# Kernel optimization log

Hardware: AMD Instinct MI355X
Metric: run time of the kernel (lower is better)

The kernel has to match this reference:

```python
import jax, jax.numpy as jnp
import numpy as np

D_MODEL = 256
GAMMA = 0.9          # ret_D is built in the torch forward but never applied to the output; kept for fidelity notes
SCALE_BASE = 512     # XPOS default
TEMP = 10000.0
TWO_PI = 2.0 * np.pi


def sine_pos_embed(x):
    """DETR-style 1D sine position embedding with an all-ones mask (as in forward).
    x: [B,T,C] -> pos: [1,T,C] (mask is [1,T] ones, so batch dim broadcasts)."""
    T, C = x.shape[1], x.shape[2]
    x_embed = jnp.arange(1, T + 1, dtype=jnp.float32)          # cumsum of ones
    x_embed = x_embed / (x_embed[-1] + 1e-6) * TWO_PI          # normalize=True
    dim_t = TEMP ** (2.0 * (jnp.arange(C) // 2).astype(jnp.float32) / C)
    pos = x_embed[:, None] / dim_t                             # [T,C]
    pos = jnp.stack([jnp.sin(pos[:, 0::2]), jnp.cos(pos[:, 1::2])], axis=2).reshape(T, C)
    return pos[None].astype(x.dtype)


def _dup_interleave(m):
    # [L, d/2] -> [L, d], columns repeated pairwise: [a,b] -> [a,a,b,b]
    return jnp.repeat(m, 2, axis=-1)


def _rotate_every_two(x):
    x1, x2 = x[..., 0::2], x[..., 1::2]
    return jnp.stack([-x2, x1], axis=-1).reshape(x.shape)


def xpos_apply(x, downscale=False):
    """RetNet XPOS rotary embedding. x: [B,L,d]."""
    L, d = x.shape[1], x.shape[2]
    half = d // 2
    scale_vec = (jnp.arange(0, d, 2, dtype=jnp.float32) + 0.4 * d) / (1.4 * d)   # [d/2]
    power = jnp.arange(L, dtype=jnp.float32) / SCALE_BASE
    scale = scale_vec[None, :] ** power[:, None]                                  # [L, d/2]
    inv_freq = 1.0 / (TEMP ** (jnp.arange(half, dtype=jnp.float32) / half))
    sinusoid = jnp.arange(L, dtype=jnp.float32)[:, None] * inv_freq[None, :]      # [L, d/2]
    sin, cos = jnp.sin(sinusoid), jnp.cos(sinusoid)
    if downscale:
        scale = 1.0 / scale
    sin_s = _dup_interleave(sin * scale)[None].astype(x.dtype)   # [1,L,d]
    cos_s = _dup_interleave(cos * scale)[None].astype(x.dtype)
    return x * cos_s + _rotate_every_two(x) * sin_s


def setup_inputs() -> dict:
    key = jax.random.key(0)
    ks = jax.random.split(key, 8)
    B, TXT, VID, D = 16, 32, 2048, D_MODEL
    S = TXT + VID
    inp = {
        "src": jax.random.normal(ks[0], (B, S, D), dtype=jnp.float32),
        "learn_vid_ret": jax.random.normal(ks[1], (VID * VID, 1), dtype=jnp.float32),
        "W_txt_Q": jax.random.normal(ks[2], (D, D), dtype=jnp.float32) / D,
        "W_txt_K": jax.random.normal(ks[3], (D, D), dtype=jnp.float32) / D,
        "W_txt_V": jax.random.normal(ks[4], (D, D), dtype=jnp.float32) / D,
        "W_vid_Q": jax.random.normal(ks[5], (D, D), dtype=jnp.float32) / D,
        "W_vid_K": jax.random.normal(ks[6], (D, D), dtype=jnp.float32) / D,
        "W_vid_V": jax.random.normal(ks[7], (D, D), dtype=jnp.float32) / D,
        "txt_length": TXT,
    }
    return inp


def reference(src, learn_vid_ret, W_txt_Q, W_txt_K, W_txt_V, W_vid_Q, W_vid_K, W_vid_V, txt_length):
    S = src.shape[1]
    vid_length = S - txt_length

    # learned retention mask over the video block
    learn_ret = jax.nn.sigmoid(learn_vid_ret.reshape(vid_length, vid_length))
    diag = jnp.eye(vid_length, dtype=src.dtype)
    video_ret = (1.0 - diag) * learn_ret
    loss_sparsity = jnp.mean(jnp.abs(video_ret))

    # full [S,S] mask: ones everywhere, sigmoid(learned) on the vid-vid block
    ret_mask = jnp.ones((S, S), dtype=src.dtype).at[txt_length:, txt_length:].set(learn_ret)

    txt_mem = src[:, :txt_length]   # [B,TXT,D]
    vid_mem = src[:, txt_length:]   # [B,VID,D]

    pos = sine_pos_embed(txt_mem)   # [1,TXT,D]
    txt_Q = (pos + txt_mem) @ W_txt_Q
    txt_K = (pos + txt_mem) @ W_txt_K
    vid_Q = xpos_apply(vid_mem @ W_vid_Q)
    vid_K = xpos_apply(vid_mem @ W_vid_K, downscale=True)

    Q = jnp.concatenate([txt_Q, vid_Q], axis=1)                  # [B,S,D]
    K = jnp.concatenate([txt_K, vid_K], axis=1)                  # [B,S,D]
    V = jnp.concatenate([txt_mem @ W_txt_V, vid_mem @ W_vid_V], axis=1)

    # retention: QK^T elementwise-masked (no softmax), then weighted V sum
    scores = jnp.einsum('bsd,btd->bst', Q, K) * ret_mask[None]   # [B,S,S]
    out = scores @ V                                             # [B,S,D]
    return out, loss_sparsity
```

## Files before the change

### kernel.cpp

```cpp
#include <hip/hip_runtime.h>

#define B_   16
#define TXT  32
#define VID  2048
#define D_   256
#define S_   2080
#define SP   2176
#define NKT  34
#define GTOT 17424

typedef unsigned short ushort_t;
typedef __attribute__((ext_vector_type(8))) short short8;
typedef __attribute__((ext_vector_type(4))) short short4v;
typedef __attribute__((ext_vector_type(4))) float f32x4;
typedef __attribute__((ext_vector_type(16))) float f32x16;

__device__ __forceinline__ ushort_t f2bf(float f) {
  unsigned u = __builtin_bit_cast(unsigned, f);
  unsigned r = (u + 0x7FFFu + ((u >> 16) & 1u)) >> 16;
  return (ushort_t)r;
}
__device__ __forceinline__ float bf2f(ushort_t h) {
  unsigned u = ((unsigned)h) << 16;
  return __builtin_bit_cast(float, u);
}

__device__ __forceinline__ void g2l16(void* lds, const void* g) {
  __builtin_amdgcn_global_load_lds(
      (const __attribute__((address_space(1))) char*)g,
      (__attribute__((address_space(3))) char*)lds, 16, 0, 0);
}

__device__ __forceinline__ f32x4 mfma16(short8 a, short8 b, f32x4 c) {
  return __builtin_amdgcn_mfma_f32_16x16x32_bf16(a, b, c, 0, 0, 0);
}
__device__ __forceinline__ f32x16 mfma32(short8 a, short8 b, f32x16 c) {
  return __builtin_amdgcn_mfma_f32_32x32x16_bf16(a, b, c, 0, 0, 0);
}


__global__ void tbl_kernel(float* __restrict__ tbl) {
  int idx = blockIdx.x * 256 + threadIdx.x;
  int n = idx >> 7, i = idx & 127;
  float invf = powf(10000.0f, -(float)i / 128.0f);
  float ang = (float)n * invf;
  float s, co;
  sincosf(ang, &s, &co);
  float sv = ((float)(2 * i) + 102.4f) / 358.4f;
  float sc = powf(sv, (float)n / 512.0f);
  float4 r;
  r.x = co * sc; r.y = s * sc; r.z = co / sc; r.w = s / sc;
  *(float4*)(tbl + (size_t)idx * 4) = r;
}

__global__ void sig_loss_kernel(const float* __restrict__ learn, ushort_t* __restrict__ sigp,
                                float* __restrict__ loss) {
  const int tid = threadIdx.x;
  const int base = (blockIdx.x * 256 + tid) * 8;
  float4 v0 = *(const float4*)(learn + base);
  float4 v1 = *(const float4*)(learn + base + 4);
  float vals[8] = {v0.x, v0.y, v0.z, v0.w, v1.x, v1.y, v1.z, v1.w};
  float acc = 0.f;
  short8 sh;
  #pragma unroll
  for (int j = 0; j < 8; ++j) {
    int idx = base + j;
    float s = 1.0f / (1.0f + expf(-vals[j]));
    sh[j] = (short)f2bf(s);
    int rr = idx >> 11, cc = idx & 2047;
    if (rr != cc) acc += s;
  }
  *(short8*)(sigp + base) = sh;
  __shared__ float red[256];
  red[tid] = acc;
  __syncthreads();
  #pragma unroll
  for (int st = 128; st > 0; st >>= 1) {
    if (tid < st) red[tid] += red[tid + st];
    __syncthreads();
  }
  if (tid == 0) atomicAdd(loss, red[0] * (1.0f / 4194304.0f));
}

__global__ void cvt_kernel(const float* __restrict__ src, ushort_t* __restrict__ srcb) {
  int i = blockIdx.x * 256 + threadIdx.x;
  int b = i >> 16;
  int rem = i & 65535;
  int row = rem >> 5, c8 = (rem & 31) * 8;
  const float* p = src + ((size_t)b * S_ + TXT + row) * D_ + c8;
  float4 v0 = *(const float4*)p;
  float4 v1 = *(const float4*)(p + 4);
  short8 h;
  h[0] = (short)f2bf(v0.x); h[1] = (short)f2bf(v0.y); h[2] = (short)f2bf(v0.z); h[3] = (short)f2bf(v0.w);
  h[4] = (short)f2bf(v1.x); h[5] = (short)f2bf(v1.y); h[6] = (short)f2bf(v1.z); h[7] = (short)f2bf(v1.w);
  *(short8*)(srcb + ((size_t)b * VID + row) * D_ + c8) = h;
}

__global__ void pad0_kernel(ushort_t* __restrict__ Qs, ushort_t* __restrict__ Ks,
                            ushort_t* __restrict__ VTs) {
  int i = blockIdx.x * 256 + threadIdx.x;
  short8 z = {0, 0, 0, 0, 0, 0, 0, 0};
  int sec = i >> 14;
  int j = i & 16383;
  int bb = j >> 10;
  int rem = j & 1023;
  size_t base = ((size_t)(bb * NKT + 32)) << 14;
  if (sec == 0) {
    int kstep = rem >> 6, ch = rem & 63;
    *(short8*)(Qs + base + kstep * 1024 + 512 + ch * 8) = z;
  } else if (sec == 1) {
    int kstep = rem >> 6, ch = rem & 63;
    *(short8*)(Ks + base + kstep * 1024 + 512 + ch * 8) = z;
  } else {
    *(short8*)(VTs + base + 8192 + rem * 8) = z;
  }
}

__global__ void wt_kernel(const float* __restrict__ Wq, const float* __restrict__ Wk,
                          const float* __restrict__ Wv, ushort_t* __restrict__ WT) {
  __shared__ float t[64][68];
  const int k0 = blockIdx.x * 64, n0 = blockIdx.y * 64, mt = blockIdx.z;
  const float* W = (mt == 0) ? Wq : (mt == 1) ? Wk : Wv;
  int tid = threadIdx.x;
  int r = tid >> 4, cq = (tid & 15) * 4;
  #pragma unroll
  for (int m = 0; m < 4; ++m) {
    int k = m * 16 + r;
    float4 v = *(const float4*)(W + (size_t)(k0 + k) * 256 + n0 + cq);
    t[k][cq] = v.x; t[k][cq + 1] = v.y; t[k][cq + 2] = v.z; t[k][cq + 3] = v.w;
  }
  __syncthreads();
  #pragma unroll
  for (int m = 0; m < 4; ++m) {
    int n = m * 16 + r;
    short4v h;
    h[0] = (short)f2bf(t[cq + 0][n]);
    h[1] = (short)f2bf(t[cq + 1][n]);
    h[2] = (short)f2bf(t[cq + 2][n]);
    h[3] = (short)f2bf(t[cq + 3][n]);
    *(short4v*)(WT + ((size_t)mt * D_ + n0 + n) * D_ + k0 + cq) = h;
  }
}

__global__ void txt_kernel(const float* __restrict__ src,
                           const float* __restrict__ Wq, const float* __restrict__ Wk,
                           const float* __restrict__ Wv,
                           ushort_t* __restrict__ Qs, ushort_t* __restrict__ Ks,
                           ushort_t* __restrict__ VTs) {
  __shared__ float a_s[8][256];
  __shared__ float x_s[8][256];
  const int tg = blockIdx.x;
  const int b  = blockIdx.y;
  const int c  = threadIdx.x;
  #pragma unroll
  for (int t = 0; t < 8; ++t) {
    int row = tg * 8 + t;
    float x = src[((size_t)b * S_ + row) * D_ + c];
    float xe = (float)(row + 1) * (6.283185307179586f / (32.0f + 1e-6f));
    int i = c >> 1;
    float dimt = powf(10000.0f, (2.0f * (float)i) / 256.0f);
    float ang = xe / dimt;
    float pv = (c & 1) ? cosf(ang) : sinf(ang);
    x_s[t][c] = x;
    a_s[t][c] = x + pv;
  }
  __syncthreads();
  float q[8] = {0,0,0,0,0,0,0,0}, k[8] = {0,0,0,0,0,0,0,0}, v[8] = {0,0,0,0,0,0,0,0};
  for (int kk = 0; kk < 256; ++kk) {
    float wq = Wq[(size_t)kk * 256 + c];
    float wk = Wk[(size_t)kk * 256 + c];
    float wv = Wv[(size_t)kk * 256 + c];
    #pragma unroll
    for (int t = 0; t < 8; ++t) {
      q[t] = fmaf(a_s[t][kk], wq, q[t]);
      k[t] = fmaf(a_s[t][kk], wk, k[t]);
      v[t] = fmaf(x_s[t][kk], wv, v[t]);
    }
  }
  #pragma unroll
  for (int t = 0; t < 8; ++t) {
    int row = tg * 8 + t;
    size_t base = ((size_t)(b * NKT)) << 14;
    size_t sub = (size_t)(c >> 4) * 1024 + row * 16 + (c & 15);
    Qs[base + sub] = f2bf(q[t]);
    Ks[base + sub] = f2bf(k[t]);
    VTs[base + (size_t)(row >> 4) * 4096 + c * 16 + (row & 15)] = f2bf(v[t]);
  }
}

template <int MODE>
__global__ __launch_bounds__(256, 2) void vid_gemm(
    const float* __restrict__ src, const ushort_t* __restrict__ srcb,
    const ushort_t* __restrict__ WT, const float* __restrict__ tbl,
    ushort_t* __restrict__ Qs, ushort_t* __restrict__ Ks, ushort_t* __restrict__ VTs) {
  __shared__ __align__(16) ushort_t ldsA[64 * 64];
  __shared__ __align__(16) ushort_t ldsB[64 * 64];

  const int rt = blockIdx.x;
  const int b  = blockIdx.y;
  const int ct = blockIdx.z;
  const int nt = ct >> 2;
  const int n0 = (ct & 3) * 64;
  const int tid = threadIdx.x;
  const int wv = tid >> 6, lane = tid & 63, l15 = lane & 15, l4 = lane >> 4;

  f32x4 acc[4];
  #pragma unroll
  for (int t2 = 0; t2 < 4; ++t2) { acc[t2][0] = 0.f; acc[t2][1] = 0.f; acc[t2][2] = 0.f; acc[t2][3] = 0.f; }

  for (int kk = 0; kk < 256; kk += 64) {
    if (MODE == 1) {
      #pragma unroll
      for (int m = 0; m < 2; ++m) {
        int p = (m * 256 + tid) * 16;
        int r = p >> 7;
        int cb = (p & 127) ^ ((r & 7) << 4);
        g2l16((char*)ldsA + p,
              (const char*)(srcb + ((size_t)b * VID + rt * 64 + r) * D_ + kk) + cb);
      }
    } else {
      #pragma unroll
      for (int m = 0; m < 4; ++m) {
        int q = m * 256 + tid;
        int r = q >> 4;
        int kc = (q & 15) * 4;
        const float4 v = *(const float4*)(src + ((size_t)b * S_ + TXT + rt * 64 + r) * D_ + kk + kc);
        short4v h;
        h[0] = (short)f2bf(v.x); h[1] = (short)f2bf(v.y);
        h[2] = (short)f2bf(v.z); h[3] = (short)f2bf(v.w);
        int off = ((r << 7) + (kc << 1)) ^ ((r & 7) << 4);
        *(short4v*)((char*)ldsA + off) = h;
      }
    }
    #pragma unroll
    for (int m = 0; m < 2; ++m) {
      int p = (m * 256 + tid) * 16;
      int nl = p >> 7;
      int c = (p & 127) ^ ((nl & 7) << 4);
      g2l16((char*)ldsB + p, (const char*)(WT + ((size_t)nt * D_ + n0 + nl) * D_ + kk) + c);
    }
    __syncthreads();
    #pragma unroll
    for (int ks = 0; ks < 2; ++ks) {
      int ar = wv * 16 + l15;
      int aoff = ((ar << 7) + ((ks * 32 + l4 * 8) << 1)) ^ ((ar & 7) << 4);
      short8 av = *(const short8*)((const char*)ldsA + aoff);
      #pragma unroll
      for (int t2 = 0; t2 < 4; ++t2) {
        int nl = t2 * 16 + l15;
        int boff = ((nl << 7) + ((ks * 32 + l4 * 8) << 1)) ^ ((nl & 7) << 4);
        short8 bv = *(const short8*)((const char*)ldsB + boff);
        acc[t2] = mfma16(av, bv, acc[t2]);
      }
    }
    __syncthreads();
  }

  const int rowl = wv * 16 + l4 * 4;
  if (nt < 2) {
    #pragma unroll
    for (int t2 = 0; t2 < 4; ++t2) {
      int c = n0 + t2 * 16 + l15;
      #pragma unroll
      for (int r = 0; r < 4; ++r) {
        int n = rt * 64 + rowl + r;
        float x = acc[t2][r];
        float xp = __shfl_xor(x, 1);
        const float4 tb = *(const float4*)(tbl + ((size_t)n * 128 + (c >> 1)) * 4);
        float cs = (nt == 0) ? tb.x : tb.z;
        float ss = (nt == 0) ? tb.y : tb.w;
        float val = (c & 1) ? fmaf(x, cs, xp * ss) : fmaf(x, cs, -xp * ss);
        int rowg = TXT + n;
        size_t idx = (((size_t)(b * NKT + (rowg >> 6))) << 14)
                   + (size_t)(c >> 4) * 1024 + (rowg & 63) * 16 + (c & 15);
        if (nt == 0) Qs[idx] = f2bf(val);
        else         Ks[idx] = f2bf(val);
      }
    }
  } else {
    #pragma unroll
    for (int t2 = 0; t2 < 4; ++t2)
      #pragma unroll
      for (int r = 0; r < 4; ++r) {
        int rr = rowl + r;
        int cc = t2 * 16 + l15;
        int off = ((rr << 7) + (cc << 1)) ^ ((rr & 7) << 4);
        *(ushort_t*)((char*)ldsA + off) = f2bf(acc[t2][r]);
      }
    __syncthreads();
    int n = tid >> 2;
    int rc = (tid & 3) * 16;
    short8 o0, o1;
    #pragma unroll
    for (int j = 0; j < 8; ++j) {
      int rr = rc + j;
      int off = ((rr << 7) + (n << 1)) ^ ((rr & 7) << 4);
      o0[j] = *(const short*)((const char*)ldsA + off);
    }
    #pragma unroll
    for (int j = 0; j < 8; ++j) {
      int rr = rc + 8 + j;
      int off = ((rr << 7) + (n << 1)) ^ ((rr & 7) << 4);
      o1[j] = *(const short*)((const char*)ldsA + off);
    }
    int d = n0 + n;
    int kvg0 = TXT + rt * 64 + rc;
    size_t base = (((size_t)(b * NKT + (kvg0 >> 6))) << 14) + ((kvg0 >> 4) & 3) * 4096 + d * 16;
    *(short8*)(VTs + base) = o0;
    *(short8*)(VTs + base + 8) = o1;
  }
}

__global__ __launch_bounds__(256) void attn_kernel(
    const ushort_t* __restrict__ Qs, const ushort_t* __restrict__ Ks,
    const ushort_t* __restrict__ VTs, const ushort_t* __restrict__ sigp,
    float* __restrict__ out) {
  __shared__ __align__(16) ushort_t Pb[4096];

  const int kblk = blockIdx.x;
  const int bs = (kblk & 7) * 128 + (kblk >> 3);
  int g = bs * 17 + (bs >> 6);
  const int gend = (bs + 1) * 17 + ((bs + 1) >> 6);

  const int tid = threadIdx.x;
  const int wid = tid >> 6, lane = tid & 63;
  const int l31 = lane & 31, l5 = lane >> 5;
  const int qh = wid >> 1, kh = wid & 1;
  const int d0 = wid * 64;
  const int qloc = qh * 32 + l31;
  const int pswz = (l31 & 7) << 4;

  int b = g / 1089, rem = g - b * 1089, qt = rem / 33, kvt = rem - qt * 33;

  f32x16 oacc[2][2];
  #pragma unroll
  for (int i2 = 0; i2 < 2; ++i2)
    #pragma unroll
    for (int j2 = 0; j2 < 2; ++j2)
      #pragma unroll
      for (int r = 0; r < 16; ++r) oacc[i2][j2][r] = 0.f;

  while (g < gend) {
    int4 mq[4];
    {
      int q = qt * 64 + qloc;
      int qc = q - TXT; qc = qc < 0 ? 0 : (qc > 2047 ? 2047 : qc);
      int kvp = kvt * 64 + kh * 32 - TXT;
      int kvc = (kvp >= 0 && kvp <= 2016) ? kvp : 0;
      const int4* mrow = (const int4*)(sigp + (size_t)qc * 2048 + kvc);
      mq[0] = mrow[0]; mq[1] = mrow[1]; mq[2] = mrow[2]; mq[3] = mrow[3];
    }

    const ushort_t* kb = Ks + (((size_t)(b * NKT + kvt)) << 14) + (kh * 32 + l31) * 16 + l5 * 8;
    const ushort_t* qb = Qs + (((size_t)(b * NKT + qt)) << 14) + qloc * 16 + l5 * 8;
    f32x16 s;
    #pragma unroll
    for (int r = 0; r < 16; ++r) s[r] = 0.f;
    __builtin_amdgcn_s_setprio(1);
    #pragma unroll
    for (int ks = 0; ks < 16; ++ks) {
      short8 kf = *(const short8*)(kb + ks * 1024);
      short8 qf = *(const short8*)(qb + ks * 1024);
      s = mfma32(kf, qf, s);
    }
    __builtin_amdgcn_s_setprio(0);

    {
      int q = qt * 64 + qloc;
      bool qv = (q >= TXT) && (q < S_);
      int kvp = kvt * 64 + kh * 32 - TXT;
      bool kvv = (kvp >= 0 && kvp <= 2016);
      bool ok = qv && kvv;
      const unsigned* mw = (const unsigned*)mq;
      #pragma unroll
      for (int t = 0; t < 4; ++t) {
        unsigned w0p, w1p;
        {
          unsigned wa = mw[4 * t + 0], wb = mw[4 * t + 2];
          unsigned w = l5 ? wb : wa;
          float m0 = ok ? bf2f((ushort_t)(w & 0xFFFFu)) : 1.0f;
          float m1 = ok ? bf2f((ushort_t)(w >> 16)) : 1.0f;
          int r = 4 * t;
          float p0 = s[r] * m0;
          float p1 = s[r + 1] * m1;
          asm("v_cvt_pk_bf16_f32 %0, %1, %2" : "=v"(w0p) : "v"(p0), "v"(p1));
        }
        {
          unsigned wa = mw[4 * t + 1], wb = mw[4 * t + 3];
          unsigned w = l5 ? wb : wa;
          float m0 = ok ? bf2f((ushort_t)(w & 0xFFFFu)) : 1.0f;
          float m1 = ok ? bf2f((ushort_t)(w >> 16)) : 1.0f;
          int r = 4 * t + 2;
          float p0 = s[r] * m0;
          float p1 = s[r + 1] * m1;
          asm("v_cvt_pk_bf16_f32 %0, %1, %2" : "=v"(w1p) : "v"(p0), "v"(p1));
        }
        int off = ((qloc << 7) + (kh << 6) + (t << 4) + (l5 << 3)) ^ pswz;
        *(uint2*)((char*)Pb + off) = make_uint2(w0p, w1p);
      }
    }

    asm volatile("s_waitcnt lgkmcnt(0)" ::: "memory");
    __builtin_amdgcn_sched_barrier(0);
    __builtin_amdgcn_s_barrier();
    __builtin_amdgcn_sched_barrier(0);

    const ushort_t* vb = VTs + (((size_t)(b * NKT + kvt)) << 14) + (size_t)d0 * 16 + l5 * 8;
    __builtin_amdgcn_s_setprio(1);
    #pragma unroll
    for (int ks = 0; ks < 4; ++ks) {
      short8 pf0 = *(const short8*)((const char*)Pb + ((l31 * 128 + ks * 32 + l5 * 16) ^ pswz));
      short8 pf1 = *(const short8*)((const char*)Pb + (((32 + l31) * 128 + ks * 32 + l5 * 16) ^ pswz));
      short8 vf0 = *(const short8*)(vb + ks * 4096 + l31 * 16);
      short8 vf1 = *(const short8*)(vb + ks * 4096 + (l31 + 32) * 16);
      oacc[0][0] = mfma32(pf0, vf0, oacc[0][0]);
      oacc[0][1] = mfma32(pf0, vf1, oacc[0][1]);
      oacc[1][0] = mfma32(pf1, vf0, oacc[1][0]);
      oacc[1][1] = mfma32(pf1, vf1, oacc[1][1]);
    }
    __builtin_amdgcn_s_setprio(0);
    asm volatile("s_waitcnt lgkmcnt(0)" ::: "memory");
    __builtin_amdgcn_sched_barrier(0);

    if (kvt == 32 || g + 1 == gend) {
      #pragma unroll
      for (int qg2 = 0; qg2 < 2; ++qg2)
        #pragma unroll
        for (int dg = 0; dg < 2; ++dg)
          #pragma unroll
          for (int r = 0; r < 16; ++r) {
            int qg = qt * 64 + qg2 * 32 + (r & 3) + 8 * (r >> 2) + 4 * l5;
            int dd = d0 + dg * 32 + l31;
            if (qg < S_)
              unsafeAtomicAdd(&out[((size_t)b * S_ + qg) * D_ + dd], oacc[qg2][dg][r]);
            oacc[qg2][dg][r] = 0.f;
          }
    }

    __builtin_amdgcn_s_barrier();
    __builtin_amdgcn_sched_barrier(0);

    ++g;
    ++kvt;
    if (kvt == 33) { kvt = 0; ++qt; if (qt == 33) { qt = 0; ++b; } }
  }
}

extern "C" void kernel_launch(void* const* d_in, const int* in_sizes, int n_in,
                              void* d_out, int out_size, void* d_ws, size_t ws_size,
                              hipStream_t stream) {
  (void)in_sizes; (void)n_in;
  const float* src   = (const float*)d_in[0];
  const float* learn = (const float*)d_in[1];
  const float* Wtq = (const float*)d_in[2];
  const float* Wtk = (const float*)d_in[3];
  const float* Wtv = (const float*)d_in[4];
  const float* Wvq = (const float*)d_in[5];
  const float* Wvk = (const float*)d_in[6];
  const float* Wvv = (const float*)d_in[7];
  float* out = (float*)d_out;

  char* ws = (char*)d_ws;
  const size_t QKV_ONE  = (size_t)B_ * SP * D_ * 2;
  const size_t QP_OFF   = 0;
  const size_t KS_OFF   = QP_OFF + QKV_ONE;
  const size_t VT_OFF   = KS_OFF + QKV_ONE;
  const size_t SIG_OFF  = VT_OFF + QKV_ONE;
  const size_t TBL_OFF  = SIG_OFF + (size_t)VID * VID * 2;
  const size_t WT_OFF   = TBL_OFF + (size_t)VID * 128 * 4 * sizeof(float);
  const size_t SRCB_OFF = WT_OFF + (size_t)3 * D_ * D_ * 2;
  const size_t NEED_SRCB = SRCB_OFF + (size_t)B_ * VID * D_ * 2;

  ushort_t* Qs   = (ushort_t*)(ws + QP_OFF);
  ushort_t* Ks   = (ushort_t*)(ws + KS_OFF);
  ushort_t* VTs  = (ushort_t*)(ws + VT_OFF);
  ushort_t* sigp = (ushort_t*)(ws + SIG_OFF);
  float*    tbl  = (float*)(ws + TBL_OFF);
  ushort_t* WT   = (ushort_t*)(ws + WT_OFF);
  ushort_t* srcb = (ushort_t*)(ws + SRCB_OFF);

  hipMemsetAsync(d_out, 0, (size_t)out_size * sizeof(float), stream);
  pad0_kernel<<<192, 256, 0, stream>>>(Qs, Ks, VTs);
  tbl_kernel<<<1024, 256, 0, stream>>>(tbl);
  sig_loss_kernel<<<2048, 256, 0, stream>>>(learn, sigp, out + (size_t)B_ * S_ * D_);
  wt_kernel<<<dim3(4, 4, 3), 256, 0, stream>>>(Wvq, Wvk, Wvv, WT);
  txt_kernel<<<dim3(4, B_), 256, 0, stream>>>(src, Wtq, Wtk, Wtv, Qs, Ks, VTs);
  if (ws_size >= NEED_SRCB) {
    cvt_kernel<<<4096, 256, 0, stream>>>(src, srcb);
    vid_gemm<1><<<dim3(32, B_, 12), 256, 0, stream>>>(src, srcb, WT, tbl, Qs, Ks, VTs);
  } else {
    vid_gemm<0><<<dim3(32, B_, 12), 256, 0, stream>>>(src, srcb, WT, tbl, Qs, Ks, VTs);
  }
  attn_kernel<<<dim3(1024), 256, 0, stream>>>(Qs, Ks, VTs, sigp, out);
}
```

Measured before the change: 356.8 us.

## Merge prep kernels, stage swizzled K tiles in LDS and prefetch next tile in attention

Five small preprocessing kernels (pad, table, sigmoid/loss, weight transpose, text projection) are folded into one launch to cut launch overhead. The K layout is XOR-swizzled on write. The attention kernel now stages each K tile into LDS with async global-to-LDS loads, keeps Q fragments in registers across kv tiles, and prefetches the next K tile, mask and Q while PV runs. The QK reduction is split into two independent accumulators, and the grid shrinks from 1024 to 768 blocks with more work each. This adds LDS use and register pressure, and relies on hand-counted vmcnt waits being correct.

```diff
diff --git a/kernel.cpp b/kernel.cpp
--- a/kernel.cpp
+++ b/kernel.cpp
@@ -39,47 +39,137 @@
 }
 
 
-__global__ void tbl_kernel(float* __restrict__ tbl) {
-  int idx = blockIdx.x * 256 + threadIdx.x;
-  int n = idx >> 7, i = idx & 127;
-  float invf = powf(10000.0f, -(float)i / 128.0f);
-  float ang = (float)n * invf;
-  float s, co;
-  sincosf(ang, &s, &co);
-  float sv = ((float)(2 * i) + 102.4f) / 358.4f;
-  float sc = powf(sv, (float)n / 512.0f);
-  float4 r;
-  r.x = co * sc; r.y = s * sc; r.z = co / sc; r.w = s / sc;
-  *(float4*)(tbl + (size_t)idx * 4) = r;
-}
-
-__global__ void sig_loss_kernel(const float* __restrict__ learn, ushort_t* __restrict__ sigp,
-                                float* __restrict__ loss) {
+__global__ void prep_kernel(const float* __restrict__ src, const float* __restrict__ learn,
+                            const float* __restrict__ Wtq, const float* __restrict__ Wtk,
+                            const float* __restrict__ Wtv,
+                            const float* __restrict__ Wvq, const float* __restrict__ Wvk,
+                            const float* __restrict__ Wvv,
+                            ushort_t* __restrict__ Qs, ushort_t* __restrict__ Ks,
+                            ushort_t* __restrict__ VTs, ushort_t* __restrict__ sigp,
+                            float* __restrict__ tbl, ushort_t* __restrict__ WT,
+                            float* __restrict__ loss) {
+  __shared__ float shf[64 * 68];
+  const int blk = blockIdx.x;
   const int tid = threadIdx.x;
-  const int base = (blockIdx.x * 256 + tid) * 8;
-  float4 v0 = *(const float4*)(learn + base);
-  float4 v1 = *(const float4*)(learn + base + 4);
-  float vals[8] = {v0.x, v0.y, v0.z, v0.w, v1.x, v1.y, v1.z, v1.w};
-  float acc = 0.f;
-  short8 sh;
-  #pragma unroll
-  for (int j = 0; j < 8; ++j) {
-    int idx = base + j;
-    float s = 1.0f / (1.0f + expf(-vals[j]));
-    sh[j] = (short)f2bf(s);
-    int rr = idx >> 11, cc = idx & 2047;
-    if (rr != cc) acc += s;
+
+  if (blk < 64) {
+    float (*a_s)[256] = (float(*)[256])shf;
+    float (*x_s)[256] = (float(*)[256])(shf + 2048);
+    const int tg = blk & 3;
+    const int b  = blk >> 2;
+    const int c  = tid;
+    #pragma unroll
+    for (int t = 0; t < 8; ++t) {
+      int row = tg * 8 + t;
+      float x = src[((size_t)b * S_ + row) * D_ + c];
+      float xe = (float)(row + 1) * (6.283185307179586f / (32.0f + 1e-6f));
+      int i = c >> 1;
+      float dimt = powf(10000.0f, (2.0f * (float)i) / 256.0f);
+      float ang = xe / dimt;
+      float pv = (c & 1) ? cosf(ang) : sinf(ang);
+      x_s[t][c] = x;
+      a_s[t][c] = x + pv;
+    }
+    __syncthreads();
+    float q[8] = {0,0,0,0,0,0,0,0}, k[8] = {0,0,0,0,0,0,0,0}, v[8] = {0,0,0,0,0,0,0,0};
+    for (int kk = 0; kk < 256; ++kk) {
+      float wq = Wtq[(size_t)kk * 256 + c];
+      float wk = Wtk[(size_t)kk * 256 + c];
+      float wv = Wtv[(size_t)kk * 256 + c];
+      #pragma unroll
+      for (int t = 0; t < 8; ++t) {
+        q[t] = fmaf(a_s[t][kk], wq, q[t]);
+        k[t] = fmaf(a_s[t][kk], wk, k[t]);
+        v[t] = fmaf(x_s[t][kk], wv, v[t]);
+      }
+    }
+    #pragma unroll
+    for (int t = 0; t < 8; ++t) {
+      int row = tg * 8 + t;
+      size_t base = ((size_t)(b * NKT)) << 14;
+      size_t sub = (size_t)(c >> 4) * 1024 + row * 16 + (c & 15);
+      Qs[base + sub] = f2bf(q[t]);
+      Ks[(base + sub) ^ (size_t)(((row >> 2) & 7) << 3)] = f2bf(k[t]);
+      VTs[base + (size_t)(row >> 4) * 4096 + c * 16 + (row & 15)] = f2bf(v[t]);
+    }
+  } else if (blk < 112) {
+    float (*t)[68] = (float(*)[68])shf;
+    const int m = blk - 64;
+    const int k0 = (m & 3) * 64, n0 = ((m >> 2) & 3) * 64, mt = m >> 4;
+    const float* W = (mt == 0) ? Wvq : (mt == 1) ? Wvk : Wvv;
+    int r = tid >> 4, cq = (tid & 15) * 4;
+    #pragma unroll
+    for (int mm = 0; mm < 4; ++mm) {
+      int k = mm * 16 + r;
+      float4 v = *(const float4*)(W + (size_t)(k0 + k) * 256 + n0 + cq);
+      t[k][cq] = v.x; t[k][cq + 1] = v.y; t[k][cq + 2] = v.z; t[k][cq + 3] = v.w;
+    }
+    __syncthreads();
+    #pragma unroll
+    for (int mm = 0; mm < 4; ++mm) {
+      int n = mm * 16 + r;
+      short4v h;
+      h[0] = (short)f2bf(t[cq + 0][n]);
+      h[1] = (short)f2bf(t[cq + 1][n]);
+      h[2] = (short)f2bf(t[cq + 2][n]);
+      h[3] = (short)f2bf(t[cq + 3][n]);
+      *(short4v*)(WT + ((size_t)mt * D_ + n0 + n) * D_ + k0 + cq) = h;
+    }
+  } else if (blk < 1136) {
+    int idx = (blk - 112) * 256 + tid;
+    int n = idx >> 7, i = idx & 127;
+    float invf = powf(10000.0f, -(float)i / 128.0f);
+    float ang = (float)n * invf;
+    float s, co;
+    sincosf(ang, &s, &co);
+    float sv = ((float)(2 * i) + 102.4f) / 358.4f;
+    float sc = powf(sv, (float)n / 512.0f);
+    float4 r;
+    r.x = co * sc; r.y = s * sc; r.z = co / sc; r.w = s / sc;
+    *(float4*)(tbl + (size_t)idx * 4) = r;
+  } else if (blk < 1328) {
+    int i = (blk - 1136) * 256 + tid;
+    short8 z = {0, 0, 0, 0, 0, 0, 0, 0};
+    int sec = i >> 14;
+    int j = i & 16383;
+    int bb = j >> 10;
+    int rem = j & 1023;
+    size_t base = ((size_t)(bb * NKT + 32)) << 14;
+    if (sec == 0) {
+      int kstep = rem >> 6, ch = rem & 63;
+      *(short8*)(Qs + base + kstep * 1024 + 512 + ch * 8) = z;
+    } else if (sec == 1) {
+      int kstep = rem >> 6, ch = rem & 63;
+      *(short8*)(Ks + base + kstep * 1024 + 512 + ch * 8) = z;
+    } else {
+      *(short8*)(VTs + base + 8192 + rem * 8) = z;
+    }
+  } else {
+    float* red = shf;
+    const int base = ((blk - 1328) * 256 + tid) * 8;
+    float4 v0 = *(const float4*)(learn + base);
+    float4 v1 = *(const float4*)(learn + base + 4);
+    float vals[8] = {v0.x, v0.y, v0.z, v0.w, v1.x, v1.y, v1.z, v1.w};
+    float acc = 0.f;
+    short8 sh;
+    #pragma unroll
+    for (int j = 0; j < 8; ++j) {
+      int idx = base + j;
+      float s = 1.0f / (1.0f + expf(-vals[j]));
+      sh[j] = (short)f2bf(s);
+      int rr = idx >> 11, cc = idx & 2047;
+      if (rr != cc) acc += s;
+    }
+    *(short8*)(sigp + base) = sh;
+    red[tid] = acc;
+    __syncthreads();
+    #pragma unroll
+    for (int st = 128; st > 0; st >>= 1) {
+      if (tid < st) red[tid] += red[tid + st];
+      __syncthreads();
+    }
+    if (tid == 0) atomicAdd(loss, red[0] * (1.0f / 4194304.0f));
   }
-  *(short8*)(sigp + base) = sh;
-  __shared__ float red[256];
-  red[tid] = acc;
-  __syncthreads();
-  #pragma unroll
-  for (int st = 128; st > 0; st >>= 1) {
-    if (tid < st) red[tid] += red[tid + st];
-    __syncthreads();
-  }
-  if (tid == 0) atomicAdd(loss, red[0] * (1.0f / 4194304.0f));
 }
 
 __global__ void cvt_kernel(const float* __restrict__ src, ushort_t* __restrict__ srcb) {
@@ -96,98 +186,6 @@
   *(short8*)(srcb + ((size_t)b * VID + row) * D_ + c8) = h;
 }
 
-__global__ void pad0_kernel(ushort_t* __restrict__ Qs, ushort_t* __restrict__ Ks,
-                            ushort_t* __restrict__ VTs) {
-  int i = blockIdx.x * 256 + threadIdx.x;
-  short8 z = {0, 0, 0, 0, 0, 0, 0, 0};
-  int sec = i >> 14;
-  int j = i & 16383;
-  int bb = j >> 10;
-  int rem = j & 1023;
-  size_t base = ((size_t)(bb * NKT + 32)) << 14;
-  if (sec == 0) {
-    int kstep = rem >> 6, ch = rem & 63;
-    *(short8*)(Qs + base + kstep * 1024 + 512 + ch * 8) = z;
-  } else if (sec == 1) {
-    int kstep = rem >> 6, ch = rem & 63;
-    *(short8*)(Ks + base + kstep * 1024 + 512 + ch * 8) = z;
-  } else {
-    *(short8*)(VTs + base + 8192 + rem * 8) = z;
-  }
-}
-
-__global__ void wt_kernel(const float* __restrict__ Wq, const float* __restrict__ Wk,
-                          const float* __restrict__ Wv, ushort_t* __restrict__ WT) {
-  __shared__ float t[64][68];
-  const int k0 = blockIdx.x * 64, n0 = blockIdx.y * 64, mt = blockIdx.z;
-  const float* W = (mt == 0) ? Wq : (mt == 1) ? Wk : Wv;
-  int tid = threadIdx.x;
-  int r = tid >> 4, cq = (tid & 15) * 4;
-  #pragma unroll
-  for (int m = 0; m < 4; ++m) {
-    int k = m * 16 + r;
-    float4 v = *(const float4*)(W + (size_t)(k0 + k) * 256 + n0 + cq);
-    t[k][cq] = v.x; t[k][cq + 1] = v.y; t[k][cq + 2] = v.z; t[k][cq + 3] = v.w;
-  }
-  __syncthreads();
-  #pragma unroll
-  for (int m = 0; m < 4; ++m) {
-    int n = m * 16 + r;
-    short4v h;
-    h[0] = (short)f2bf(t[cq + 0][n]);
-    h[1] = (short)f2bf(t[cq + 1][n]);
-    h[2] = (short)f2bf(t[cq + 2][n]);
-    h[3] = (short)f2bf(t[cq + 3][n]);
-    *(short4v*)(WT + ((size_t)mt * D_ + n0 + n) * D_ + k0 + cq) = h;
-  }
-}
-
-__global__ void txt_kernel(const float* __restrict__ src,
-                           const float* __restrict__ Wq, const float* __restrict__ Wk,
-                           const float* __restrict__ Wv,
-                           ushort_t* __restrict__ Qs, ushort_t* __restrict__ Ks,
-                           ushort_t* __restrict__ VTs) {
-  __shared__ float a_s[8][256];
-  __shared__ float x_s[8][256];
-  const int tg = blockIdx.x;
-  const int b  = blockIdx.y;
-  const int c  = threadIdx.x;
-  #pragma unroll
-  for (int t = 0; t < 8; ++t) {
-    int row = tg * 8 + t;
-    float x = src[((size_t)b * S_ + row) * D_ + c];
-    float xe = (float)(row + 1) * (6.283185307179586f / (32.0f + 1e-6f));
-    int i = c >> 1;
-    float dimt = powf(10000.0f, (2.0f * (float)i) / 256.0f);
-    float ang = xe / dimt;
-    float pv = (c & 1) ? cosf(ang) : sinf(ang);
-    x_s[t][c] = x;
-    a_s[t][c] = x + pv;
-  }
-  __syncthreads();
-  float q[8] = {0,0,0,0,0,0,0,0}, k[8] = {0,0,0,0,0,0,0,0}, v[8] = {0,0,0,0,0,0,0,0};
-  for (int kk = 0; kk < 256; ++kk) {
-    float wq = Wq[(size_t)kk * 256 + c];
-    float wk = Wk[(size_t)kk * 256 + c];
-    float wv = Wv[(size_t)kk * 256 + c];
-    #pragma unroll
-    for (int t = 0; t < 8; ++t) {
-      q[t] = fmaf(a_s[t][kk], wq, q[t]);
-      k[t] = fmaf(a_s[t][kk], wk, k[t]);
-      v[t] = fmaf(x_s[t][kk], wv, v[t]);
-    }
-  }
-  #pragma unroll
-  for (int t = 0; t < 8; ++t) {
-    int row = tg * 8 + t;
-    size_t base = ((size_t)(b * NKT)) << 14;
-    size_t sub = (size_t)(c >> 4) * 1024 + row * 16 + (c & 15);
-    Qs[base + sub] = f2bf(q[t]);
-    Ks[base + sub] = f2bf(k[t]);
-    VTs[base + (size_t)(row >> 4) * 4096 + c * 16 + (row & 15)] = f2bf(v[t]);
-  }
-}
-
 template <int MODE>
 __global__ __launch_bounds__(256, 2) void vid_gemm(
     const float* __restrict__ src, const ushort_t* __restrict__ srcb,
@@ -274,7 +272,7 @@
         size_t idx = (((size_t)(b * NKT + (rowg >> 6))) << 14)
                    + (size_t)(c >> 4) * 1024 + (rowg & 63) * 16 + (c & 15);
         if (nt == 0) Qs[idx] = f2bf(val);
-        else         Ks[idx] = f2bf(val);
+        else         Ks[idx ^ (size_t)(((rowg >> 2) & 7) << 3)] = f2bf(val);
       }
     }
   } else {
@@ -315,12 +313,13 @@
     const ushort_t* __restrict__ Qs, const ushort_t* __restrict__ Ks,
     const ushort_t* __restrict__ VTs, const ushort_t* __restrict__ sigp,
     float* __restrict__ out) {
+  __shared__ __align__(16) ushort_t Kb[16384];
   __shared__ __align__(16) ushort_t Pb[4096];
 
   const int kblk = blockIdx.x;
-  const int bs = (kblk & 7) * 128 + (kblk >> 3);
-  int g = bs * 17 + (bs >> 6);
-  const int gend = (bs + 1) * 17 + ((bs + 1) >> 6);
+  const int bs = (kblk & 7) * 96 + (kblk >> 3);
+  int g = bs * 22 + (bs < 528 ? bs : 528);
+  const int gend = g + 22 + (bs < 528 ? 1 : 0);
 
   const int tid = threadIdx.x;
   const int wid = tid >> 6, lane = tid & 63;
@@ -329,8 +328,33 @@
   const int d0 = wid * 64;
   const int qloc = qh * 32 + l31;
   const int pswz = (l31 & 7) << 4;
+  const int krbase = kh * 32 + l31;
+  const int kxor = ((krbase >> 2) & 7) << 4;
+  const int krow = krbase * 32 + l5 * 16;
 
   int b = g / 1089, rem = g - b * 1089, qt = rem / 33, kvt = rem - qt * 33;
+
+  short8 qf[16];
+  int4 mq[4];
+
+  auto ldq = [&](int bb, int qq) {
+    const ushort_t* qb = Qs + (((size_t)(bb * NKT + qq)) << 14) + qloc * 16 + l5 * 8;
+    #pragma unroll
+    for (int ks = 0; ks < 16; ++ks) qf[ks] = *(const short8*)(qb + ks * 1024);
+  };
+  auto ldmask = [&](int qq, int tt) {
+    int q = qq * 64 + qloc;
+    int qc = q - TXT; qc = qc < 0 ? 0 : (qc > 2047 ? 2047 : qc);
+    int kvp = tt * 64 + kh * 32 - TXT;
+    int kvc = (kvp >= 0 && kvp <= 2016) ? kvp : 0;
+    const int4* mrow = (const int4*)(sigp + (size_t)qc * 2048 + kvc);
+    mq[0] = mrow[0]; mq[1] = mrow[1]; mq[2] = mrow[2]; mq[3] = mrow[3];
+  };
+  auto stageK = [&](int bb, int tt) {
+    const char* src = (const char*)Ks + (((size_t)(bb * NKT + tt)) << 15);
+    #pragma unroll
+    for (int m = 0; m < 8; ++m) { int s2 = m * 256 + tid; g2l16((char*)Kb + s2 * 16, src + s2 * 16); }
+  };
 
   f32x16 oacc[2][2];
   #pragma unroll
@@ -340,28 +364,29 @@
       #pragma unroll
       for (int r = 0; r < 16; ++r) oacc[i2][j2][r] = 0.f;
 
+  stageK(b, kvt);
+  ldmask(qt, kvt);
+  ldq(b, qt);
+  asm volatile("s_waitcnt vmcnt(0)" ::: "memory");
+  __builtin_amdgcn_sched_barrier(0);
+  __builtin_amdgcn_s_barrier();
+  __builtin_amdgcn_sched_barrier(0);
+
   while (g < gend) {
-    int4 mq[4];
-    {
-      int q = qt * 64 + qloc;
-      int qc = q - TXT; qc = qc < 0 ? 0 : (qc > 2047 ? 2047 : qc);
-      int kvp = kvt * 64 + kh * 32 - TXT;
-      int kvc = (kvp >= 0 && kvp <= 2016) ? kvp : 0;
-      const int4* mrow = (const int4*)(sigp + (size_t)qc * 2048 + kvc);
-      mq[0] = mrow[0]; mq[1] = mrow[1]; mq[2] = mrow[2]; mq[3] = mrow[3];
-    }
-
-    const ushort_t* kb = Ks + (((size_t)(b * NKT + kvt)) << 14) + (kh * 32 + l31) * 16 + l5 * 8;
-    const ushort_t* qb = Qs + (((size_t)(b * NKT + qt)) << 14) + qloc * 16 + l5 * 8;
-    f32x16 s;
-    #pragma unroll
-    for (int r = 0; r < 16; ++r) s[r] = 0.f;
+    int n1_b = b, n1_q = qt, n1_k = kvt + 1;
+    if (n1_k == 33) { n1_k = 0; ++n1_q; if (n1_q == 33) { n1_q = 0; ++n1_b; } }
+    const bool last = (g + 1 == gend);
+
+    f32x16 s0, s1;
+    #pragma unroll
+    for (int r = 0; r < 16; ++r) { s0[r] = 0.f; s1[r] = 0.f; }
     __builtin_amdgcn_s_setprio(1);
     #pragma unroll
-    for (int ks = 0; ks < 16; ++ks) {
-      short8 kf = *(const short8*)(kb + ks * 1024);
-      short8 qf = *(const short8*)(qb + ks * 1024);
-      s = mfma32(kf, qf, s);
+    for (int ks = 0; ks < 8; ++ks) {
+      short8 ka = *(const short8*)((const char*)Kb + ((ks * 2048 + krow) ^ kxor));
+      short8 kc = *(const short8*)((const char*)Kb + (((ks + 8) * 2048 + krow) ^ kxor));
+      s0 = mfma32(ka, qf[ks], s0);
+      s1 = mfma32(kc, qf[ks + 8], s1);
     }
     __builtin_amdgcn_s_setprio(0);
 
@@ -381,8 +406,8 @@
           float m0 = ok ? bf2f((ushort_t)(w & 0xFFFFu)) : 1.0f;
           float m1 = ok ? bf2f((ushort_t)(w >> 16)) : 1.0f;
           int r = 4 * t;
-          float p0 = s[r] * m0;
-          float p1 = s[r + 1] * m1;
+          float p0 = (s0[r] + s1[r]) * m0;
+          float p1 = (s0[r + 1] + s1[r + 1]) * m1;
           asm("v_cvt_pk_bf16_f32 %0, %1, %2" : "=v"(w0p) : "v"(p0), "v"(p1));
         }
         {
@@ -391,8 +416,8 @@
           float m0 = ok ? bf2f((ushort_t)(w & 0xFFFFu)) : 1.0f;
           float m1 = ok ? bf2f((ushort_t)(w >> 16)) : 1.0f;
           int r = 4 * t + 2;
-          float p0 = s[r] * m0;
-          float p1 = s[r + 1] * m1;
+          float p0 = (s0[r] + s1[r]) * m0;
+          float p1 = (s0[r + 1] + s1[r + 1]) * m1;
           asm("v_cvt_pk_bf16_f32 %0, %1, %2" : "=v"(w1p) : "v"(p0), "v"(p1));
         }
         int off = ((qloc << 7) + (kh << 6) + (t << 4) + (l5 << 3)) ^ pswz;
@@ -405,14 +430,16 @@
     __builtin_amdgcn_s_barrier();
     __builtin_amdgcn_sched_barrier(0);
 
+    if (!last) stageK(n1_b, n1_k);
+
     const ushort_t* vb = VTs + (((size_t)(b * NKT + kvt)) << 14) + (size_t)d0 * 16 + l5 * 8;
     __builtin_amdgcn_s_setprio(1);
     #pragma unroll
     for (int ks = 0; ks < 4; ++ks) {
+      short8 vf0 = *(const short8*)(vb + ks * 4096 + l31 * 16);
+      short8 vf1 = *(const short8*)(vb + ks * 4096 + (l31 + 32) * 16);
       short8 pf0 = *(const short8*)((const char*)Pb + ((l31 * 128 + ks * 32 + l5 * 16) ^ pswz));
       short8 pf1 = *(const short8*)((const char*)Pb + (((32 + l31) * 128 + ks * 32 + l5 * 16) ^ pswz));
-      short8 vf0 = *(const short8*)(vb + ks * 4096 + l31 * 16);
-      short8 vf1 = *(const short8*)(vb + ks * 4096 + (l31 + 32) * 16);
       oacc[0][0] = mfma32(pf0, vf0, oacc[0][0]);
       oacc[0][1] = mfma32(pf0, vf1, oacc[0][1]);
       oacc[1][0] = mfma32(pf1, vf0, oacc[1][0]);
@@ -422,7 +449,7 @@
     asm volatile("s_waitcnt lgkmcnt(0)" ::: "memory");
     __builtin_amdgcn_sched_barrier(0);
 
-    if (kvt == 32 || g + 1 == gend) {
+    if (kvt == 32 || last) {
       #pragma unroll
       for (int qg2 = 0; qg2 < 2; ++qg2)
         #pragma unroll
@@ -437,12 +464,20 @@
           }
     }
 
+    if (!last) {
+      ldmask(n1_q, n1_k);
+      if (n1_q != qt || n1_b != b) {
+        ldq(n1_b, n1_q);
+        asm volatile("s_waitcnt vmcnt(20)" ::: "memory");
+      } else {
+        asm volatile("s_waitcnt vmcnt(4)" ::: "memory");
+      }
+    }
+    __builtin_amdgcn_sched_barrier(0);
     __builtin_amdgcn_s_barrier();
     __builtin_amdgcn_sched_barrier(0);
 
-    ++g;
-    ++kvt;
-    if (kvt == 33) { kvt = 0; ++qt; if (qt == 33) { qt = 0; ++b; } }
+    b = n1_b; qt = n1_q; kvt = n1_k; ++g;
   }
 }
 
@@ -478,18 +513,16 @@
   float*    tbl  = (float*)(ws + TBL_OFF);
   ushort_t* WT   = (ushort_t*)(ws + WT_OFF);
   ushort_t* srcb = (ushort_t*)(ws + SRCB_OFF);
+  float*    loss = out + (size_t)B_ * S_ * D_;
 
   hipMemsetAsync(d_out, 0, (size_t)out_size * sizeof(float), stream);
-  pad0_kernel<<<192, 256, 0, stream>>>(Qs, Ks, VTs);
-  tbl_kernel<<<1024, 256, 0, stream>>>(tbl);
-  sig_loss_kernel<<<2048, 256, 0, stream>>>(learn, sigp, out + (size_t)B_ * S_ * D_);
-  wt_kernel<<<dim3(4, 4, 3), 256, 0, stream>>>(Wvq, Wvk, Wvv, WT);
-  txt_kernel<<<dim3(4, B_), 256, 0, stream>>>(src, Wtq, Wtk, Wtv, Qs, Ks, VTs);
+  prep_kernel<<<3376, 256, 0, stream>>>(src, learn, Wtq, Wtk, Wtv, Wvq, Wvk, Wvv,
+                                        Qs, Ks, VTs, sigp, tbl, WT, loss);
   if (ws_size >= NEED_SRCB) {
     cvt_kernel<<<4096, 256, 0, stream>>>(src, srcb);
     vid_gemm<1><<<dim3(32, B_, 12), 256, 0, stream>>>(src, srcb, WT, tbl, Qs, Ks, VTs);
   } else {
     vid_gemm<0><<<dim3(32, B_, 12), 256, 0, stream>>>(src, srcb, WT, tbl, Qs, Ks, VTs);
   }
-  attn_kernel<<<dim3(1024), 256, 0, stream>>>(Qs, Ks, VTs, sigp, out);
-}
+  attn_kernel<<<dim3(768), 256, 0, stream>>>(Qs, Ks, VTs, sigp, out);
+}
```

Result: no change. 354.0 us (-0.8%).
